# Kernel tuning notes

Measured on AMD Instinct MI355X. Metric: run time of the kernel, lower is better.

## Reference

```python
import jax, jax.numpy as jnp
import numpy as np

N_NODES = 20000
N_EDGES = 320000
NFEAT, NHID, NCLASS = 512, 256, 64


def setup_inputs() -> dict:
    key = jax.random.key(0)
    ks = jax.random.split(key, 8)
    x = jax.random.normal(ks[0], (N_NODES, NFEAT), dtype=jnp.float32)
    edge_index = jax.random.randint(ks[1], (2, N_EDGES), 0, N_NODES, dtype=jnp.int32)
    edge_weight = jax.random.uniform(ks[2], (N_EDGES,), dtype=jnp.float32)
    W1 = jax.random.normal(ks[3], (NFEAT, NHID), dtype=jnp.float32) / np.sqrt(NFEAT)
    b1 = jax.random.normal(ks[4], (NHID,), dtype=jnp.float32) * 0.01
    W2 = jax.random.normal(ks[5], (NHID, NCLASS), dtype=jnp.float32) / np.sqrt(NHID)
    b2 = jax.random.normal(ks[6], (NCLASS,), dtype=jnp.float32) * 0.01
    return {"x": x, "edge_index": edge_index, "edge_weight": edge_weight,
            "W1": W1, "b1": b1, "W2": W2, "b2": b2}


def reference(x, edge_index, edge_weight, W1, b1, W2, b2):
    # GraphConvolution: out = adj @ (x @ W) + b, adj given as weighted edge list
    row, col = edge_index[0], edge_index[1]
    n = x.shape[0]

    def gcn(h, W, b):
        support = h @ W                                   # [N, d_out]
        msgs = edge_weight[:, None] * support[col]        # gather: [E, d_out]
        agg = jax.ops.segment_sum(msgs, row, num_segments=n)  # scatter-add
        return agg + b

    h = jax.nn.selu(gcn(x, W1, b1))        # [N, nhid]
    h = jax.nn.selu(gcn(h, W2, b2))        # [N, nclass]
    pooled = jax.nn.selu(jnp.mean(h, axis=0, keepdims=True))  # [1, nclass]
    # dropout is identity at eval time
    return jax.nn.log_softmax(pooled, axis=1)
```

## Files before the change

kernel.cpp:

```cpp
#include <hip/hip_runtime.h>
#include <math.h>

#define N_NODES 20000
#define N_EDGES 320000
#define NFEAT 512
#define NHID 256
#define NCLASS 64

typedef __attribute__((ext_vector_type(8))) short bf16x8;
typedef __attribute__((ext_vector_type(4))) float f32x4;

__device__ __forceinline__ float selu_f(float x) {
    const float alpha = 1.6732632423543772f;
    const float scale = 1.0507009873554805f;
    return x > 0.f ? scale * x : scale * alpha * (expf(x) - 1.f);
}

__device__ __forceinline__ short f2bf(float f) {
    unsigned u = __builtin_bit_cast(unsigned, f);
    unsigned r = (u + 0x7FFFu + ((u >> 16) & 1u)) >> 16;
    return (short)r;
}

__device__ __forceinline__ float bf2f(unsigned short b) {
    unsigned u = ((unsigned)b) << 16;
    return __builtin_bit_cast(float, u);
}

__global__ void k_cast_x(const float* __restrict__ in, short* __restrict__ out, int n8) {
    int i = blockIdx.x * blockDim.x + threadIdx.x;
    if (i >= n8) return;
    const float4* p = (const float4*)(in + (size_t)i * 8);
    float4 a = p[0], b = p[1];
    bf16x8 o;
    o[0] = f2bf(a.x); o[1] = f2bf(a.y); o[2] = f2bf(a.z); o[3] = f2bf(a.w);
    o[4] = f2bf(b.x); o[5] = f2bf(b.y); o[6] = f2bf(b.z); o[7] = f2bf(b.w);
    *(bf16x8*)(out + (size_t)i * 8) = o;
}

__global__ void k_cast_t(const float* __restrict__ in, short* __restrict__ out, int K, int N) {
    int t = blockIdx.x * blockDim.x + threadIdx.x;
    if (t >= K * N) return;
    int n = t / K, k = t % K;
    out[t] = f2bf(in[(size_t)k * N + n]);
}

__global__ void k_count(const int* __restrict__ row, int* __restrict__ counts) {
    int e = blockIdx.x * blockDim.x + threadIdx.x;
    if (e < N_EDGES) atomicAdd(&counts[row[e]], 1);
}

__global__ void k_scan(const int* __restrict__ counts, int* __restrict__ row_ptr,
                       int* __restrict__ write_ptr) {
    __shared__ int wsum[16];
    __shared__ int carry;
    int tid = threadIdx.x;
    int wave = tid >> 6, lane = tid & 63;
    if (tid == 0) carry = 0;
    __syncthreads();
    for (int base = 0; base < N_NODES; base += 1024) {
        int i = base + tid;
        int v = (i < N_NODES) ? counts[i] : 0;
        int s = v;
        #pragma unroll
        for (int d = 1; d < 64; d <<= 1) {
            int t = __shfl_up(s, d);
            if (lane >= d) s += t;
        }
        if (lane == 63) wsum[wave] = s;
        __syncthreads();
        if (wave == 0) {
            int t = (lane < 16) ? wsum[lane] : 0;
            #pragma unroll
            for (int d = 1; d < 16; d <<= 1) {
                int u = __shfl_up(t, d);
                if (lane >= d) t += u;
            }
            if (lane < 16) wsum[lane] = t;
        }
        __syncthreads();
        int woff = (wave == 0) ? 0 : wsum[wave - 1];
        int excl = carry + woff + s - v;
        if (i < N_NODES) { row_ptr[i] = excl; write_ptr[i] = excl; }
        int total = wsum[15];
        __syncthreads();
        if (tid == 0) carry += total;
        __syncthreads();
    }
    if (tid == 0) row_ptr[N_NODES] = carry;
}

__global__ void k_scatter(const int* __restrict__ row, const int* __restrict__ col,
                          const float* __restrict__ w, int* __restrict__ write_ptr,
                          int2* __restrict__ epack) {
    int e = blockIdx.x * blockDim.x + threadIdx.x;
    if (e < N_EDGES) {
        int r = row[e];
        int pos = atomicAdd(&write_ptr[r], 1);
        epack[pos] = make_int2(col[e], __builtin_bit_cast(int, w[e]));
    }
}

template<int BM, int BN, int MREP, int NREP>
__global__ __launch_bounds__(256) void k_gemm_bf16(
    const short* __restrict__ A, const short* __restrict__ Bt,
    short* __restrict__ C, int M, int N, int K)
{
    constexpr int BK = 32;
    constexpr int LDT = BK + 8;
    __shared__ short As[BM * LDT];
    __shared__ short Bs[BN * LDT];
    const int tid = threadIdx.x;
    const int lane = tid & 63;
    const int w = tid >> 6;
    const int wr = w >> 1, wc = w & 1;
    const int m0 = blockIdx.x * BM, n0 = blockIdx.y * BN;

    f32x4 acc[MREP][NREP] = {};

    constexpr int A_ITER = BM * BK / 8 / 256;
    constexpr int B_ITER = BN * BK / 8 / 256;

    for (int kt = 0; kt < K; kt += BK) {
        #pragma unroll
        for (int it = 0; it < A_ITER; ++it) {
            int idx = tid + it * 256;
            int r = idx >> 2, seg = idx & 3;
            int gr = m0 + r; if (gr >= M) gr = M - 1;
            bf16x8 v = *(const bf16x8*)(A + (size_t)gr * K + kt + seg * 8);
            *(bf16x8*)(As + r * LDT + seg * 8) = v;
        }
        #pragma unroll
        for (int it = 0; it < B_ITER; ++it) {
            int idx = tid + it * 256;
            int r = idx >> 2, seg = idx & 3;
            bf16x8 v = *(const bf16x8*)(Bt + (size_t)(n0 + r) * K + kt + seg * 8);
            *(bf16x8*)(Bs + r * LDT + seg * 8) = v;
        }
        __syncthreads();
        bf16x8 a[MREP], b[NREP];
        #pragma unroll
        for (int m = 0; m < MREP; ++m)
            a[m] = *(const bf16x8*)(As + (wr * (BM / 2) + m * 16 + (lane & 15)) * LDT + (lane >> 4) * 8);
        #pragma unroll
        for (int n = 0; n < NREP; ++n)
            b[n] = *(const bf16x8*)(Bs + (wc * (BN / 2) + n * 16 + (lane & 15)) * LDT + (lane >> 4) * 8);
        #pragma unroll
        for (int m = 0; m < MREP; ++m)
            #pragma unroll
            for (int n = 0; n < NREP; ++n)
                acc[m][n] = __builtin_amdgcn_mfma_f32_16x16x32_bf16(a[m], b[n], acc[m][n], 0, 0, 0);
        __syncthreads();
    }
    #pragma unroll
    for (int m = 0; m < MREP; ++m) {
        #pragma unroll
        for (int n = 0; n < NREP; ++n) {
            #pragma unroll
            for (int r = 0; r < 4; ++r) {
                int grow = m0 + wr * (BM / 2) + m * 16 + (lane >> 4) * 4 + r;
                int gcol = n0 + wc * (BN / 2) + n * 16 + (lane & 15);
                if (grow < M) C[(size_t)grow * N + gcol] = f2bf(acc[m][n][r]);
            }
        }
    }
}

__global__ __launch_bounds__(256) void k_agg1(const short* __restrict__ support,
                                              const int* __restrict__ row_ptr,
                                              const int2* __restrict__ epack,
                                              const float* __restrict__ b1,
                                              short* __restrict__ h1) {
    int wid = (blockIdx.x * 256 + threadIdx.x) >> 6;
    int lane = threadIdx.x & 63;
    if (wid >= N_NODES) return;
    int e0 = row_ptr[wid], e1 = row_ptr[wid + 1];
    float a0[4] = {}, a1[4] = {}, a2[4] = {}, a3[4] = {};
    int e = e0;
    for (; e + 4 <= e1; e += 4) {
        int2 m0 = epack[e + 0], m1 = epack[e + 1], m2 = epack[e + 2], m3 = epack[e + 3];
        ushort4 v0 = *(const ushort4*)(support + (size_t)m0.x * NHID + lane * 4);
        ushort4 v1 = *(const ushort4*)(support + (size_t)m1.x * NHID + lane * 4);
        ushort4 v2 = *(const ushort4*)(support + (size_t)m2.x * NHID + lane * 4);
        ushort4 v3 = *(const ushort4*)(support + (size_t)m3.x * NHID + lane * 4);
        float w0 = __builtin_bit_cast(float, m0.y), w1 = __builtin_bit_cast(float, m1.y);
        float w2 = __builtin_bit_cast(float, m2.y), w3 = __builtin_bit_cast(float, m3.y);
        a0[0] = fmaf(w0, bf2f(v0.x), a0[0]); a0[1] = fmaf(w0, bf2f(v0.y), a0[1]);
        a0[2] = fmaf(w0, bf2f(v0.z), a0[2]); a0[3] = fmaf(w0, bf2f(v0.w), a0[3]);
        a1[0] = fmaf(w1, bf2f(v1.x), a1[0]); a1[1] = fmaf(w1, bf2f(v1.y), a1[1]);
        a1[2] = fmaf(w1, bf2f(v1.z), a1[2]); a1[3] = fmaf(w1, bf2f(v1.w), a1[3]);
        a2[0] = fmaf(w2, bf2f(v2.x), a2[0]); a2[1] = fmaf(w2, bf2f(v2.y), a2[1]);
        a2[2] = fmaf(w2, bf2f(v2.z), a2[2]); a2[3] = fmaf(w2, bf2f(v2.w), a2[3]);
        a3[0] = fmaf(w3, bf2f(v3.x), a3[0]); a3[1] = fmaf(w3, bf2f(v3.y), a3[1]);
        a3[2] = fmaf(w3, bf2f(v3.z), a3[2]); a3[3] = fmaf(w3, bf2f(v3.w), a3[3]);
    }
    for (; e < e1; ++e) {
        int2 m = epack[e];
        float wgt = __builtin_bit_cast(float, m.y);
        ushort4 v = *(const ushort4*)(support + (size_t)m.x * NHID + lane * 4);
        a0[0] = fmaf(wgt, bf2f(v.x), a0[0]); a0[1] = fmaf(wgt, bf2f(v.y), a0[1]);
        a0[2] = fmaf(wgt, bf2f(v.z), a0[2]); a0[3] = fmaf(wgt, bf2f(v.w), a0[3]);
    }
    ushort4 o;
    o.x = (unsigned short)f2bf(selu_f(a0[0] + a1[0] + a2[0] + a3[0] + b1[lane * 4 + 0]));
    o.y = (unsigned short)f2bf(selu_f(a0[1] + a1[1] + a2[1] + a3[1] + b1[lane * 4 + 1]));
    o.z = (unsigned short)f2bf(selu_f(a0[2] + a1[2] + a2[2] + a3[2] + b1[lane * 4 + 2]));
    o.w = (unsigned short)f2bf(selu_f(a0[3] + a1[3] + a2[3] + a3[3] + b1[lane * 4 + 3]));
    *(ushort4*)(h1 + (size_t)wid * NHID + lane * 4) = o;
}

#define AGG2_NU 2
#define AGG2_WAVES (N_NODES / AGG2_NU)
__global__ __launch_bounds__(256) void k_agg2(const short* __restrict__ support2,
                                              const int* __restrict__ row_ptr,
                                              const int2* __restrict__ epack,
                                              const float* __restrict__ b2,
                                              float* __restrict__ partial) {
    int wid = (blockIdx.x * 256 + threadIdx.x) >> 6;
    int lane = threadIdx.x & 63;
    float bias = b2[lane];
    float local = 0.f;
    #pragma unroll
    for (int q = 0; q < AGG2_NU; ++q) {
        int node = wid * AGG2_NU + q;
        int e0 = row_ptr[node], e1 = row_ptr[node + 1];
        float s0 = 0.f, s1 = 0.f, s2 = 0.f, s3 = 0.f;
        int e = e0;
        for (; e + 4 <= e1; e += 4) {
            int2 m0 = epack[e + 0], m1 = epack[e + 1], m2 = epack[e + 2], m3 = epack[e + 3];
            float v0 = bf2f((unsigned short)support2[(size_t)m0.x * NCLASS + lane]);
            float v1 = bf2f((unsigned short)support2[(size_t)m1.x * NCLASS + lane]);
            float v2 = bf2f((unsigned short)support2[(size_t)m2.x * NCLASS + lane]);
            float v3 = bf2f((unsigned short)support2[(size_t)m3.x * NCLASS + lane]);
            s0 = fmaf(__builtin_bit_cast(float, m0.y), v0, s0);
            s1 = fmaf(__builtin_bit_cast(float, m1.y), v1, s1);
            s2 = fmaf(__builtin_bit_cast(float, m2.y), v2, s2);
            s3 = fmaf(__builtin_bit_cast(float, m3.y), v3, s3);
        }
        for (; e < e1; ++e) {
            int2 m = epack[e];
            s0 = fmaf(__builtin_bit_cast(float, m.y),
                      bf2f((unsigned short)support2[(size_t)m.x * NCLASS + lane]), s0);
        }
        local += selu_f(s0 + s1 + s2 + s3 + bias);
    }
    partial[(size_t)wid * NCLASS + lane] = local;
}

__global__ __launch_bounds__(256) void k_reduce(const float* __restrict__ partial,
                                                float* __restrict__ gsum) {
    int c = blockIdx.x, tid = threadIdx.x;
    float s = 0.f;
    for (int i = tid; i < AGG2_WAVES; i += 256)
        s += partial[(size_t)i * NCLASS + c];
    #pragma unroll
    for (int off = 32; off >= 1; off >>= 1) s += __shfl_xor(s, off);
    __shared__ float red[4];
    if ((tid & 63) == 0) red[tid >> 6] = s;
    __syncthreads();
    if (tid == 0) gsum[c] = red[0] + red[1] + red[2] + red[3];
}

__global__ void k_final(const float* __restrict__ gsum, float* __restrict__ out) {
    int lane = threadIdx.x;
    float v = gsum[lane] * (1.0f / N_NODES);
    v = selu_f(v);
    float m = v;
    #pragma unroll
    for (int off = 32; off >= 1; off >>= 1) m = fmaxf(m, __shfl_xor(m, off));
    float ex = expf(v - m);
    float s = ex;
    #pragma unroll
    for (int off = 32; off >= 1; off >>= 1) s += __shfl_xor(s, off);
    out[lane] = v - m - logf(s);
}

extern "C" void kernel_launch(void* const* d_in, const int* in_sizes, int n_in,
                              void* d_out, int out_size, void* d_ws, size_t ws_size,
                              hipStream_t stream) {
    const float* x  = (const float*)d_in[0];
    const int* ei   = (const int*)d_in[1];
    const float* ew = (const float*)d_in[2];
    const float* W1 = (const float*)d_in[3];
    const float* b1 = (const float*)d_in[4];
    const float* W2 = (const float*)d_in[5];
    const float* b2 = (const float*)d_in[6];
    float* out = (float*)d_out;
    const int* e_row = ei;
    const int* e_col = ei + N_EDGES;

    char* p = (char*)d_ws;
    short* xb       = (short*)p;  p += (size_t)N_NODES * NFEAT * 2;
    short* w1t      = (short*)p;  p += (size_t)NHID * NFEAT * 2;
    short* w2t      = (short*)p;  p += (size_t)NCLASS * NHID * 2;
    short* support1 = (short*)p;  p += (size_t)N_NODES * NHID * 2;
    int* counts     = (int*)p;    p += (size_t)N_NODES * 4;
    int* row_ptr    = (int*)p;    p += (size_t)(N_NODES + 1) * 4;
    int* write_ptr  = (int*)p;    p += (size_t)N_NODES * 4;
    int2* epack     = (int2*)p;   p += (size_t)N_EDGES * 8;
    float* partial  = (float*)p;  p += (size_t)AGG2_WAVES * NCLASS * 4;
    float* gsum     = (float*)p;  p += 64 * 4;
    short* h1       = xb;
    short* support2 = support1;

    hipMemsetAsync(counts, 0, (size_t)N_NODES * 4, stream);

    k_count<<<(N_EDGES + 255) / 256, 256, 0, stream>>>(e_row, counts);
    k_scan<<<1, 1024, 0, stream>>>(counts, row_ptr, write_ptr);
    k_scatter<<<(N_EDGES + 255) / 256, 256, 0, stream>>>(e_row, e_col, ew, write_ptr, epack);

    k_cast_x<<<(N_NODES * NFEAT / 8 + 255) / 256, 256, 0, stream>>>(x, xb, N_NODES * NFEAT / 8);
    k_cast_t<<<(NFEAT * NHID + 255) / 256, 256, 0, stream>>>(W1, w1t, NFEAT, NHID);
    k_cast_t<<<(NHID * NCLASS + 255) / 256, 256, 0, stream>>>(W2, w2t, NHID, NCLASS);

    k_gemm_bf16<128, 128, 4, 4><<<dim3((N_NODES + 127) / 128, NHID / 128), 256, 0, stream>>>(
        xb, w1t, support1, N_NODES, NHID, NFEAT);
    k_agg1<<<(N_NODES * 64 + 255) / 256, 256, 0, stream>>>(support1, row_ptr, epack, b1, h1);

    k_gemm_bf16<64, 64, 2, 2><<<dim3((N_NODES + 63) / 64, NCLASS / 64), 256, 0, stream>>>(
        h1, w2t, support2, N_NODES, NCLASS, NHID);
    k_agg2<<<(AGG2_WAVES * 64) / 256, 256, 0, stream>>>(support2, row_ptr, epack, b2, partial);
    k_reduce<<<NCLASS, 256, 0, stream>>>(partial, gsum);

    k_final<<<1, 64, 0, stream>>>(gsum, out);
}
```

Baseline: 244.3 us.

## Fuse x cast into GEMM, merge weight casts, single-pass scan, fuse final reduction

The fp32-to-bf16 cast of x now happens inside the first GEMM's tile load, which removes the separate cast kernel and its round trip through a bf16 copy of x. The GEMM gains a BK parameter, with BK=64 for layer 1. The two weight-transpose casts are merged into one launch. The scan becomes a single pass with 20 elements per thread instead of a serial loop over 1024-element chunks. agg2 reduces its four waves in shared memory, and the final reduction, SELU and log-softmax are fused into one kernel. Together these cut launch count and memory traffic, at the cost of fp32 loads and conversions inside the GEMM loop and a larger LDS tile.

```diff
diff --git a/kernel.cpp b/kernel.cpp
--- a/kernel.cpp
+++ b/kernel.cpp
@@ -27,22 +27,19 @@
     return __builtin_bit_cast(float, u);
 }
 
-__global__ void k_cast_x(const float* __restrict__ in, short* __restrict__ out, int n8) {
-    int i = blockIdx.x * blockDim.x + threadIdx.x;
-    if (i >= n8) return;
-    const float4* p = (const float4*)(in + (size_t)i * 8);
-    float4 a = p[0], b = p[1];
-    bf16x8 o;
-    o[0] = f2bf(a.x); o[1] = f2bf(a.y); o[2] = f2bf(a.z); o[3] = f2bf(a.w);
-    o[4] = f2bf(b.x); o[5] = f2bf(b.y); o[6] = f2bf(b.z); o[7] = f2bf(b.w);
-    *(bf16x8*)(out + (size_t)i * 8) = o;
-}
-
-__global__ void k_cast_t(const float* __restrict__ in, short* __restrict__ out, int K, int N) {
+__global__ void k_cast_w(const float* __restrict__ W1, const float* __restrict__ W2,
+                         short* __restrict__ w1t, short* __restrict__ w2t) {
     int t = blockIdx.x * blockDim.x + threadIdx.x;
-    if (t >= K * N) return;
-    int n = t / K, k = t % K;
-    out[t] = f2bf(in[(size_t)k * N + n]);
+    if (t < NFEAT * NHID) {
+        int n = t / NFEAT, k = t % NFEAT;
+        w1t[t] = f2bf(W1[(size_t)k * NHID + n]);
+    } else {
+        int u = t - NFEAT * NHID;
+        if (u < NHID * NCLASS) {
+            int n = u / NHID, k = u % NHID;
+            w2t[u] = f2bf(W2[(size_t)k * NCLASS + n]);
+        }
+    }
 }
 
 __global__ void k_count(const int* __restrict__ row, int* __restrict__ counts) {
@@ -50,44 +47,46 @@
     if (e < N_EDGES) atomicAdd(&counts[row[e]], 1);
 }
 
-__global__ void k_scan(const int* __restrict__ counts, int* __restrict__ row_ptr,
-                       int* __restrict__ write_ptr) {
+__global__ __launch_bounds__(1024) void k_scan(const int* __restrict__ counts,
+                                               int* __restrict__ row_ptr,
+                                               int* __restrict__ write_ptr) {
     __shared__ int wsum[16];
-    __shared__ int carry;
-    int tid = threadIdx.x;
-    int wave = tid >> 6, lane = tid & 63;
-    if (tid == 0) carry = 0;
+    int tid = threadIdx.x, lane = tid & 63, wave = tid >> 6;
+    int base = tid * 20;
+    int v[20];
+    int s = 0;
+    #pragma unroll
+    for (int j = 0; j < 20; ++j) {
+        int i = base + j;
+        int c = (i < N_NODES) ? counts[i] : 0;
+        v[j] = s;
+        s += c;
+    }
+    int ws = s;
+    #pragma unroll
+    for (int d = 1; d < 64; d <<= 1) {
+        int t = __shfl_up(ws, d);
+        if (lane >= d) ws += t;
+    }
+    if (lane == 63) wsum[wave] = ws;
     __syncthreads();
-    for (int base = 0; base < N_NODES; base += 1024) {
-        int i = base + tid;
-        int v = (i < N_NODES) ? counts[i] : 0;
-        int s = v;
-        #pragma unroll
-        for (int d = 1; d < 64; d <<= 1) {
-            int t = __shfl_up(s, d);
-            if (lane >= d) s += t;
-        }
-        if (lane == 63) wsum[wave] = s;
-        __syncthreads();
-        if (wave == 0) {
-            int t = (lane < 16) ? wsum[lane] : 0;
-            #pragma unroll
-            for (int d = 1; d < 16; d <<= 1) {
-                int u = __shfl_up(t, d);
-                if (lane >= d) t += u;
-            }
-            if (lane < 16) wsum[lane] = t;
-        }
-        __syncthreads();
-        int woff = (wave == 0) ? 0 : wsum[wave - 1];
-        int excl = carry + woff + s - v;
-        if (i < N_NODES) { row_ptr[i] = excl; write_ptr[i] = excl; }
-        int total = wsum[15];
-        __syncthreads();
-        if (tid == 0) carry += total;
-        __syncthreads();
-    }
-    if (tid == 0) row_ptr[N_NODES] = carry;
+    if (wave == 0) {
+        int t = (lane < 16) ? wsum[lane] : 0;
+        #pragma unroll
+        for (int d = 1; d < 16; d <<= 1) {
+            int u = __shfl_up(t, d);
+            if (lane >= d) t += u;
+        }
+        if (lane < 16) wsum[lane] = t;
+    }
+    __syncthreads();
+    int off = (wave ? wsum[wave - 1] : 0) + (ws - s);
+    #pragma unroll
+    for (int j = 0; j < 20; ++j) {
+        int i = base + j;
+        if (i < N_NODES) { row_ptr[i] = off + v[j]; write_ptr[i] = off + v[j]; }
+    }
+    if (tid == 0) row_ptr[N_NODES] = wsum[15];
 }
 
 __global__ void k_scatter(const int* __restrict__ row, const int* __restrict__ col,
@@ -101,12 +100,11 @@
     }
 }
 
-template<int BM, int BN, int MREP, int NREP>
+template<int BM, int BN, int BK, int MREP, int NREP, bool AFP32>
 __global__ __launch_bounds__(256) void k_gemm_bf16(
-    const short* __restrict__ A, const short* __restrict__ Bt,
+    const void* __restrict__ Av, const short* __restrict__ Bt,
     short* __restrict__ C, int M, int N, int K)
 {
-    constexpr int BK = 32;
     constexpr int LDT = BK + 8;
     __shared__ short As[BM * LDT];
     __shared__ short Bs[BN * LDT];
@@ -115,41 +113,54 @@
     const int w = tid >> 6;
     const int wr = w >> 1, wc = w & 1;
     const int m0 = blockIdx.x * BM, n0 = blockIdx.y * BN;
+    constexpr int SEGS = BK / 8;
+    constexpr int A_ITER = BM * SEGS / 256;
+    constexpr int B_ITER = BN * SEGS / 256;
 
     f32x4 acc[MREP][NREP] = {};
-
-    constexpr int A_ITER = BM * BK / 8 / 256;
-    constexpr int B_ITER = BN * BK / 8 / 256;
 
     for (int kt = 0; kt < K; kt += BK) {
         #pragma unroll
         for (int it = 0; it < A_ITER; ++it) {
             int idx = tid + it * 256;
-            int r = idx >> 2, seg = idx & 3;
+            int r = idx / SEGS, seg = idx % SEGS;
             int gr = m0 + r; if (gr >= M) gr = M - 1;
-            bf16x8 v = *(const bf16x8*)(A + (size_t)gr * K + kt + seg * 8);
-            *(bf16x8*)(As + r * LDT + seg * 8) = v;
+            bf16x8 o;
+            if constexpr (AFP32) {
+                const float* ap = (const float*)Av + (size_t)gr * K + kt + seg * 8;
+                float4 p0 = *(const float4*)ap, p1 = *(const float4*)(ap + 4);
+                o[0] = f2bf(p0.x); o[1] = f2bf(p0.y); o[2] = f2bf(p0.z); o[3] = f2bf(p0.w);
+                o[4] = f2bf(p1.x); o[5] = f2bf(p1.y); o[6] = f2bf(p1.z); o[7] = f2bf(p1.w);
+            } else {
+                o = *(const bf16x8*)((const short*)Av + (size_t)gr * K + kt + seg * 8);
+            }
+            *(bf16x8*)(As + r * LDT + seg * 8) = o;
         }
         #pragma unroll
         for (int it = 0; it < B_ITER; ++it) {
             int idx = tid + it * 256;
-            int r = idx >> 2, seg = idx & 3;
-            bf16x8 v = *(const bf16x8*)(Bt + (size_t)(n0 + r) * K + kt + seg * 8);
-            *(bf16x8*)(Bs + r * LDT + seg * 8) = v;
+            int r = idx / SEGS, seg = idx % SEGS;
+            *(bf16x8*)(Bs + r * LDT + seg * 8) =
+                *(const bf16x8*)(Bt + (size_t)(n0 + r) * K + kt + seg * 8);
         }
         __syncthreads();
-        bf16x8 a[MREP], b[NREP];
-        #pragma unroll
-        for (int m = 0; m < MREP; ++m)
-            a[m] = *(const bf16x8*)(As + (wr * (BM / 2) + m * 16 + (lane & 15)) * LDT + (lane >> 4) * 8);
-        #pragma unroll
-        for (int n = 0; n < NREP; ++n)
-            b[n] = *(const bf16x8*)(Bs + (wc * (BN / 2) + n * 16 + (lane & 15)) * LDT + (lane >> 4) * 8);
-        #pragma unroll
-        for (int m = 0; m < MREP; ++m)
+        #pragma unroll
+        for (int ks = 0; ks < BK / 32; ++ks) {
+            bf16x8 a[MREP], b[NREP];
+            #pragma unroll
+            for (int m = 0; m < MREP; ++m)
+                a[m] = *(const bf16x8*)(As + (wr * (BM / 2) + m * 16 + (lane & 15)) * LDT
+                                        + ks * 32 + (lane >> 4) * 8);
             #pragma unroll
             for (int n = 0; n < NREP; ++n)
-                acc[m][n] = __builtin_amdgcn_mfma_f32_16x16x32_bf16(a[m], b[n], acc[m][n], 0, 0, 0);
+                b[n] = *(const bf16x8*)(Bs + (wc * (BN / 2) + n * 16 + (lane & 15)) * LDT
+                                        + ks * 32 + (lane >> 4) * 8);
+            #pragma unroll
+            for (int m = 0; m < MREP; ++m)
+                #pragma unroll
+                for (int n = 0; n < NREP; ++n)
+                    acc[m][n] = __builtin_amdgcn_mfma_f32_16x16x32_bf16(a[m], b[n], acc[m][n], 0, 0, 0);
+        }
         __syncthreads();
     }
     #pragma unroll
@@ -209,20 +220,19 @@
     *(ushort4*)(h1 + (size_t)wid * NHID + lane * 4) = o;
 }
 
-#define AGG2_NU 2
-#define AGG2_WAVES (N_NODES / AGG2_NU)
+#define AGG2_BLOCKS (N_NODES / 8)
 __global__ __launch_bounds__(256) void k_agg2(const short* __restrict__ support2,
                                               const int* __restrict__ row_ptr,
                                               const int2* __restrict__ epack,
                                               const float* __restrict__ b2,
                                               float* __restrict__ partial) {
-    int wid = (blockIdx.x * 256 + threadIdx.x) >> 6;
-    int lane = threadIdx.x & 63;
+    __shared__ float bsum[4][64];
+    int tid = threadIdx.x, lane = tid & 63, wave = tid >> 6;
     float bias = b2[lane];
     float local = 0.f;
     #pragma unroll
-    for (int q = 0; q < AGG2_NU; ++q) {
-        int node = wid * AGG2_NU + q;
+    for (int q = 0; q < 2; ++q) {
+        int node = blockIdx.x * 8 + wave * 2 + q;
         int e0 = row_ptr[node], e1 = row_ptr[node + 1];
         float s0 = 0.f, s1 = 0.f, s2 = 0.f, s3 = 0.f;
         int e = e0;
@@ -244,35 +254,36 @@
         }
         local += selu_f(s0 + s1 + s2 + s3 + bias);
     }
-    partial[(size_t)wid * NCLASS + lane] = local;
-}
-
-__global__ __launch_bounds__(256) void k_reduce(const float* __restrict__ partial,
-                                                float* __restrict__ gsum) {
-    int c = blockIdx.x, tid = threadIdx.x;
+    bsum[wave][lane] = local;
+    __syncthreads();
+    if (tid < 64)
+        partial[(size_t)blockIdx.x * 64 + tid] =
+            bsum[0][tid] + bsum[1][tid] + bsum[2][tid] + bsum[3][tid];
+}
+
+__global__ __launch_bounds__(1024) void k_final_red(const float* __restrict__ partial,
+                                                    float* __restrict__ out) {
+    __shared__ float red[16][64];
+    int tid = threadIdx.x, c = tid & 63, sl = tid >> 6;
     float s = 0.f;
-    for (int i = tid; i < AGG2_WAVES; i += 256)
-        s += partial[(size_t)i * NCLASS + c];
-    #pragma unroll
-    for (int off = 32; off >= 1; off >>= 1) s += __shfl_xor(s, off);
-    __shared__ float red[4];
-    if ((tid & 63) == 0) red[tid >> 6] = s;
+    for (int i = sl; i < AGG2_BLOCKS; i += 16)
+        s += partial[(size_t)i * 64 + c];
+    red[sl][c] = s;
     __syncthreads();
-    if (tid == 0) gsum[c] = red[0] + red[1] + red[2] + red[3];
-}
-
-__global__ void k_final(const float* __restrict__ gsum, float* __restrict__ out) {
-    int lane = threadIdx.x;
-    float v = gsum[lane] * (1.0f / N_NODES);
-    v = selu_f(v);
-    float m = v;
-    #pragma unroll
-    for (int off = 32; off >= 1; off >>= 1) m = fmaxf(m, __shfl_xor(m, off));
-    float ex = expf(v - m);
-    float s = ex;
-    #pragma unroll
-    for (int off = 32; off >= 1; off >>= 1) s += __shfl_xor(s, off);
-    out[lane] = v - m - logf(s);
+    if (tid < 64) {
+        float tot = 0.f;
+        #pragma unroll
+        for (int k = 0; k < 16; ++k) tot += red[k][c];
+        float v = selu_f(tot * (1.0f / N_NODES));
+        float m = v;
+        #pragma unroll
+        for (int off = 32; off >= 1; off >>= 1) m = fmaxf(m, __shfl_xor(m, off));
+        float ex = expf(v - m);
+        float ssum = ex;
+        #pragma unroll
+        for (int off = 32; off >= 1; off >>= 1) ssum += __shfl_xor(ssum, off);
+        out[c] = v - m - logf(ssum);
+    }
 }
 
 extern "C" void kernel_launch(void* const* d_in, const int* in_sizes, int n_in,
@@ -290,17 +301,15 @@
     const int* e_col = ei + N_EDGES;
 
     char* p = (char*)d_ws;
-    short* xb       = (short*)p;  p += (size_t)N_NODES * NFEAT * 2;
     short* w1t      = (short*)p;  p += (size_t)NHID * NFEAT * 2;
     short* w2t      = (short*)p;  p += (size_t)NCLASS * NHID * 2;
     short* support1 = (short*)p;  p += (size_t)N_NODES * NHID * 2;
+    short* h1       = (short*)p;  p += (size_t)N_NODES * NHID * 2;
     int* counts     = (int*)p;    p += (size_t)N_NODES * 4;
     int* row_ptr    = (int*)p;    p += (size_t)(N_NODES + 1) * 4;
     int* write_ptr  = (int*)p;    p += (size_t)N_NODES * 4;
     int2* epack     = (int2*)p;   p += (size_t)N_EDGES * 8;
-    float* partial  = (float*)p;  p += (size_t)AGG2_WAVES * NCLASS * 4;
-    float* gsum     = (float*)p;  p += 64 * 4;
-    short* h1       = xb;
+    float* partial  = (float*)p;  p += (size_t)AGG2_BLOCKS * 64 * 4;
     short* support2 = support1;
 
     hipMemsetAsync(counts, 0, (size_t)N_NODES * 4, stream);
@@ -309,18 +318,16 @@
     k_scan<<<1, 1024, 0, stream>>>(counts, row_ptr, write_ptr);
     k_scatter<<<(N_EDGES + 255) / 256, 256, 0, stream>>>(e_row, e_col, ew, write_ptr, epack);
 
-    k_cast_x<<<(N_NODES * NFEAT / 8 + 255) / 256, 256, 0, stream>>>(x, xb, N_NODES * NFEAT / 8);
-    k_cast_t<<<(NFEAT * NHID + 255) / 256, 256, 0, stream>>>(W1, w1t, NFEAT, NHID);
-    k_cast_t<<<(NHID * NCLASS + 255) / 256, 256, 0, stream>>>(W2, w2t, NHID, NCLASS);
-
-    k_gemm_bf16<128, 128, 4, 4><<<dim3((N_NODES + 127) / 128, NHID / 128), 256, 0, stream>>>(
-        xb, w1t, support1, N_NODES, NHID, NFEAT);
+    k_cast_w<<<(NFEAT * NHID + NHID * NCLASS + 255) / 256, 256, 0, stream>>>(W1, W2, w1t, w2t);
+
+    k_gemm_bf16<128, 128, 64, 4, 4, true>
+        <<<dim3((N_NODES + 127) / 128, NHID / 128), 256, 0, stream>>>(
+            x, w1t, support1, N_NODES, NHID, NFEAT);
     k_agg1<<<(N_NODES * 64 + 255) / 256, 256, 0, stream>>>(support1, row_ptr, epack, b1, h1);
 
-    k_gemm_bf16<64, 64, 2, 2><<<dim3((N_NODES + 63) / 64, NCLASS / 64), 256, 0, stream>>>(
-        h1, w2t, support2, N_NODES, NCLASS, NHID);
-    k_agg2<<<(AGG2_WAVES * 64) / 256, 256, 0, stream>>>(support2, row_ptr, epack, b2, partial);
-    k_reduce<<<NCLASS, 256, 0, stream>>>(partial, gsum);
-
-    k_final<<<1, 64, 0, stream>>>(gsum, out);
-}
+    k_gemm_bf16<64, 64, 32, 2, 2, false>
+        <<<dim3((N_NODES + 63) / 64, NCLASS / 64), 256, 0, stream>>>(
+            h1, w2t, support2, N_NODES, NCLASS, NHID);
+    k_agg2<<<AGG2_BLOCKS, 256, 0, stream>>>(support2, row_ptr, epack, b2, partial);
+    k_final_red<<<1, 1024, 0, stream>>>(partial, out);
+}
```

Result: slower. 264.8 us (+8.4%).
